# Kernel optimization log

Measured on AMD Instinct MI355X. Metric: run time of the kernel, lower is better.

## Reference

```python
import jax, jax.numpy as jnp
import numpy as np

NUM_EXPERTS = 8
TOP_K = 2
N_EMBD = 1024
D_FFN = 2048  # 4*n_embd//top_k, already multiple of block_size=128


def setup_inputs() -> dict:
    key = jax.random.key(0)
    k1, k2, k3, k4 = jax.random.split(key, 4)
    x = jax.random.normal(k1, (4, 2048, N_EMBD), dtype=jnp.float32)
    router_w = jax.random.normal(k2, (NUM_EXPERTS, N_EMBD), dtype=jnp.float32) * 0.02
    w1 = jax.random.normal(k3, (N_EMBD, D_FFN * NUM_EXPERTS), dtype=jnp.float32) * 0.02
    w2 = jax.random.normal(k4, (D_FFN * NUM_EXPERTS, N_EMBD), dtype=jnp.float32) * 0.02
    return {"x": x, "router_w": router_w, "w1": w1, "w2": w2}


def reference(x, router_w, w1, w2):
    B, T, D = x.shape
    xf = x.reshape(B * T, D)                       # [N, d]
    N = B * T

    # Router: softmax over experts, then top-k selection and renormalization.
    logits = xf @ router_w.T                       # [N, E]
    probs = jax.nn.softmax(logits, axis=-1)
    top_v, top_i = jax.lax.top_k(probs, TOP_K)     # [N, k]
    top_v = top_v / jnp.sum(top_v, axis=-1, keepdims=True)  # norm_topk_prob=True

    # Dense [N, E] routing-weight matrix (zero for non-selected experts).
    gate = jnp.zeros((N, NUM_EXPERTS), dtype=x.dtype)
    gate = gate.at[jnp.arange(N)[:, None], top_i].set(top_v)

    w1r = w1.reshape(D, NUM_EXPERTS, D_FFN)        # expert-major column blocks
    w2r = w2.reshape(NUM_EXPERTS, D_FFN, D)

    out = jnp.zeros((N, D), dtype=x.dtype)
    for e in range(NUM_EXPERTS):
        h = jax.nn.gelu(xf @ w1r[:, e, :], approximate=False)  # [N, f]
        out = out + gate[:, e:e + 1] * (h @ w2r[e])
    return out.reshape(B, T, D)
```

## Files before the change

### kernel.cpp

```cpp
#include <hip/hip_runtime.h>
#include <hip/hip_bf16.h>
#include <cstdint>
#include <cstddef>

#define NE 8
#define N_TOK 8192
#define D_EMB 1024
#define D_FFN 2048

#define BM 128
#define BN 128
#define BK 32

typedef __attribute__((ext_vector_type(8))) short short8;
typedef __attribute__((ext_vector_type(4))) float f32x4;

__device__ __forceinline__ unsigned short f2bf(float f) {
  union { float f; unsigned int u; } c; c.f = f;
  unsigned int u = c.u;
  unsigned int r = u + 0x7FFFu + ((u >> 16) & 1u);
  return (unsigned short)(r >> 16);
}

__device__ __forceinline__ void gll16(const void* g, void* l) {
  __builtin_amdgcn_global_load_lds((const __attribute__((address_space(1))) void*)g,
                                   (__attribute__((address_space(3))) void*)l, 16, 0, 0);
}

__global__ __launch_bounds__(256) void router_k(const float* __restrict__ x,
                                                const float* __restrict__ rw,
                                                int* __restrict__ ti,
                                                float* __restrict__ tg,
                                                ushort* __restrict__ xb) {
  int w = threadIdx.x >> 6, lane = threadIdx.x & 63;
  int n = blockIdx.x * 4 + w;
  const float4* x4 = (const float4*)(x + (size_t)n * D_EMB);
  ushort4* xb4 = (ushort4*)(xb + (size_t)n * D_EMB);
  const float4* r4 = (const float4*)rw;
  float acc[NE];
#pragma unroll
  for (int e = 0; e < NE; ++e) acc[e] = 0.f;
#pragma unroll
  for (int c = 0; c < 4; ++c) {
    float4 xv = x4[c * 64 + lane];
    ushort4 o;
    o.x = f2bf(xv.x); o.y = f2bf(xv.y); o.z = f2bf(xv.z); o.w = f2bf(xv.w);
    xb4[c * 64 + lane] = o;
#pragma unroll
    for (int e = 0; e < NE; ++e) {
      float4 wv = r4[e * 256 + c * 64 + lane];
      acc[e] += xv.x * wv.x + xv.y * wv.y + xv.z * wv.z + xv.w * wv.w;
    }
  }
#pragma unroll
  for (int e = 0; e < NE; ++e) {
    float v = acc[e];
#pragma unroll
    for (int off = 32; off >= 1; off >>= 1) v += __shfl_xor(v, off);
    acc[e] = v;
  }
  if (lane == 0) {
    int e0 = 0; float v0 = acc[0];
#pragma unroll
    for (int e = 1; e < NE; ++e) if (acc[e] > v0) { v0 = acc[e]; e0 = e; }
    int e1 = -1; float v1 = -1e30f;
#pragma unroll
    for (int e = 0; e < NE; ++e) if (e != e0 && acc[e] > v1) { v1 = acc[e]; e1 = e; }
    float p1 = expf(v1 - v0);
    float g0 = 1.f / (1.f + p1);
    float g1 = p1 * g0;
    ti[2 * n] = e0; ti[2 * n + 1] = e1;
    tg[2 * n] = g0; tg[2 * n + 1] = g1;
  }
}

__global__ __launch_bounds__(256) void hist_k(const int* __restrict__ ti,
                                              int* __restrict__ counts) {
  __shared__ int lc[NE];
  if (threadIdx.x < NE) lc[threadIdx.x] = 0;
  __syncthreads();
  int s = blockIdx.x * 512 + threadIdx.x;
  atomicAdd(&lc[ti[s]], 1);
  atomicAdd(&lc[ti[s + 256]], 1);
  __syncthreads();
  if (threadIdx.x < NE) atomicAdd(&counts[threadIdx.x], lc[threadIdx.x]);
}

__global__ void prefix_k(const int* __restrict__ counts, int* __restrict__ bases,
                         int* __restrict__ cursor) {
  if (threadIdx.x == 0) {
    int s = 0;
    for (int e = 0; e < NE; ++e) { bases[e] = s; cursor[e] = s; s += counts[e]; }
  }
}

__global__ __launch_bounds__(256) void scatter_k(const int* __restrict__ ti,
                                                 const float* __restrict__ tg,
                                                 int* __restrict__ cursor,
                                                 int* __restrict__ tok,
                                                 float* __restrict__ gate) {
  __shared__ int lc[NE], lb[NE];
  if (threadIdx.x < NE) lc[threadIdx.x] = 0;
  __syncthreads();
  int s = blockIdx.x * 256 + threadIdx.x;
  int e = ti[s];
  float g = tg[s];
  int loc = atomicAdd(&lc[e], 1);
  __syncthreads();
  if (threadIdx.x < NE) lb[threadIdx.x] = atomicAdd(&cursor[threadIdx.x], lc[threadIdx.x]);
  __syncthreads();
  int pos = lb[e] + loc;
  tok[pos] = s >> 1;
  gate[pos] = g;
}

__global__ __launch_bounds__(256) void transpose_bf_k(const float* __restrict__ src,
                                                      ushort* __restrict__ dst,
                                                      int R, int C) {
  __shared__ ushort t[32][33];
  int bx = blockIdx.x, by = blockIdx.y;
  int rl = threadIdx.x >> 3, q = threadIdx.x & 7;
  float4 v = *(const float4*)&src[(size_t)(by * 32 + rl) * C + bx * 32 + q * 4];
  t[rl][q * 4 + 0] = f2bf(v.x);
  t[rl][q * 4 + 1] = f2bf(v.y);
  t[rl][q * 4 + 2] = f2bf(v.z);
  t[rl][q * 4 + 3] = f2bf(v.w);
  __syncthreads();
  ushort4 o;
  o.x = t[q * 4 + 0][rl];
  o.y = t[q * 4 + 1][rl];
  o.z = t[q * 4 + 2][rl];
  o.w = t[q * 4 + 3][rl];
  *(ushort4*)&dst[(size_t)(bx * 32 + rl) * R + by * 32 + q * 4] = o;
}

__global__ __launch_bounds__(256) void gemm1_k(const ushort* __restrict__ xb,
                                               const ushort* __restrict__ w1t,
                                               const int* __restrict__ counts,
                                               const int* __restrict__ bases,
                                               const int* __restrict__ tok,
                                               ushort* __restrict__ h) {
  int bid = blockIdx.x;
  int e = bid >> 10;
  int rem = bid & 1023;
  int mt = rem >> 4, nt = rem & 15;
  int count = counts[e];
  if (mt * BM >= count) return;
  int base = bases[e];

  __shared__ ushort Al[BM * BK];
  __shared__ ushort Bl[BN * BK];

  int tid = threadIdx.x;
  int w = tid >> 6, lane = tid & 63;

  const ushort* aptr[2]; const ushort* bptr[2];
  ushort* alds[2]; ushort* blds[2];
#pragma unroll
  for (int j = 0; j < 2; ++j) {
    int rl = w * 32 + j * 16 + (lane >> 2);
    int pr = min(base + mt * BM + rl, base + count - 1);
    int t = tok[pr];
    aptr[j] = xb + (size_t)t * D_EMB + (lane & 3) * 8;
    int c = e * D_FFN + nt * BN + rl;
    bptr[j] = w1t + (size_t)c * D_EMB + (lane & 3) * 8;
    alds[j] = Al + (w * 32 + j * 16) * BK;
    blds[j] = Bl + (w * 32 + j * 16) * BK;
  }

  f32x4 zero = {0.f, 0.f, 0.f, 0.f};
  f32x4 acc[4][4];
#pragma unroll
  for (int i = 0; i < 4; ++i)
#pragma unroll
    for (int j = 0; j < 4; ++j) acc[i][j] = zero;

  int wm = w >> 1, wn = w & 1;
  const int arow = (wm * 64 + (lane & 15)) * BK + (lane >> 4) * 8;
  const int brow = (wn * 64 + (lane & 15)) * BK + (lane >> 4) * 8;

  for (int ks = 0; ks < D_EMB / BK; ++ks) {
    __syncthreads();
#pragma unroll
    for (int j = 0; j < 2; ++j) {
      gll16(aptr[j], alds[j]);
      gll16(bptr[j], blds[j]);
      aptr[j] += BK; bptr[j] += BK;
    }
    __syncthreads();
    short8 a[4], b[4];
#pragma unroll
    for (int i = 0; i < 4; ++i) a[i] = *(const short8*)&Al[arow + i * 16 * BK];
#pragma unroll
    for (int j = 0; j < 4; ++j) b[j] = *(const short8*)&Bl[brow + j * 16 * BK];
#pragma unroll
    for (int i = 0; i < 4; ++i)
#pragma unroll
      for (int j = 0; j < 4; ++j)
        acc[i][j] = __builtin_amdgcn_mfma_f32_16x16x32_bf16(a[i], b[j], acc[i][j], 0, 0, 0);
  }

  int r0 = mt * BM + wm * 64, c0 = nt * BN + wn * 64;
#pragma unroll
  for (int i = 0; i < 4; ++i) {
#pragma unroll
    for (int q = 0; q < 4; ++q) {
      int row = r0 + i * 16 + (lane >> 4) * 4 + q;
      if (row < count) {
        size_t hb = (size_t)(base + row) * D_FFN;
#pragma unroll
        for (int j = 0; j < 4; ++j) {
          float v = acc[i][j][q];
          v = 0.5f * v * (1.f + erff(v * 0.70710678118654752f));
          h[hb + c0 + j * 16 + (lane & 15)] = f2bf(v);
        }
      }
    }
  }
}

__global__ __launch_bounds__(256) void gemm2_k(const ushort* __restrict__ h,
                                               const ushort* __restrict__ w2t,
                                               const int* __restrict__ counts,
                                               const int* __restrict__ bases,
                                               const int* __restrict__ tok,
                                               const float* __restrict__ gate,
                                               float* __restrict__ out) {
  int bid = blockIdx.x;
  int e = bid >> 9;
  int rem = bid & 511;
  int mt = rem >> 3, nt = rem & 7;
  int count = counts[e];
  if (mt * BM >= count) return;
  int base = bases[e];

  __shared__ ushort Al[BM * BK];
  __shared__ ushort Bl[BN * BK];

  int tid = threadIdx.x;
  int w = tid >> 6, lane = tid & 63;

  const ushort* aptr[2]; const ushort* bptr[2];
  ushort* alds[2]; ushort* blds[2];
#pragma unroll
  for (int j = 0; j < 2; ++j) {
    int rl = w * 32 + j * 16 + (lane >> 2);
    int pr = min(base + mt * BM + rl, base + count - 1);
    aptr[j] = h + (size_t)pr * D_FFN + (lane & 3) * 8;
    int d = nt * BN + rl;
    bptr[j] = w2t + (size_t)d * (NE * D_FFN) + e * D_FFN + (lane & 3) * 8;
    alds[j] = Al + (w * 32 + j * 16) * BK;
    blds[j] = Bl + (w * 32 + j * 16) * BK;
  }

  f32x4 zero = {0.f, 0.f, 0.f, 0.f};
  f32x4 acc[4][4];
#pragma unroll
  for (int i = 0; i < 4; ++i)
#pragma unroll
    for (int j = 0; j < 4; ++j) acc[i][j] = zero;

  int wm = w >> 1, wn = w & 1;
  const int arow = (wm * 64 + (lane & 15)) * BK + (lane >> 4) * 8;
  const int brow = (wn * 64 + (lane & 15)) * BK + (lane >> 4) * 8;

  for (int ks = 0; ks < D_FFN / BK; ++ks) {
    __syncthreads();
#pragma unroll
    for (int j = 0; j < 2; ++j) {
      gll16(aptr[j], alds[j]);
      gll16(bptr[j], blds[j]);
      aptr[j] += BK; bptr[j] += BK;
    }
    __syncthreads();
    short8 a[4], b[4];
#pragma unroll
    for (int i = 0; i < 4; ++i) a[i] = *(const short8*)&Al[arow + i * 16 * BK];
#pragma unroll
    for (int j = 0; j < 4; ++j) b[j] = *(const short8*)&Bl[brow + j * 16 * BK];
#pragma unroll
    for (int i = 0; i < 4; ++i)
#pragma unroll
      for (int j = 0; j < 4; ++j)
        acc[i][j] = __builtin_amdgcn_mfma_f32_16x16x32_bf16(a[i], b[j], acc[i][j], 0, 0, 0);
  }

  int r0 = mt * BM + wm * 64, c0 = nt * BN + wn * 64;
#pragma unroll
  for (int i = 0; i < 4; ++i) {
#pragma unroll
    for (int q = 0; q < 4; ++q) {
      int row = r0 + i * 16 + (lane >> 4) * 4 + q;
      if (row < count) {
        int pr = base + row;
        int t = tok[pr];
        float g = gate[pr];
        size_t ob = (size_t)t * D_EMB;
#pragma unroll
        for (int j = 0; j < 4; ++j) {
          atomicAdd(&out[ob + c0 + j * 16 + (lane & 15)], g * acc[i][j][q]);
        }
      }
    }
  }
}

extern "C" void kernel_launch(void* const* d_in, const int* in_sizes, int n_in,
                              void* d_out, int out_size, void* d_ws, size_t ws_size,
                              hipStream_t stream) {
  const float* x  = (const float*)d_in[0];
  const float* rw = (const float*)d_in[1];
  const float* w1 = (const float*)d_in[2];
  const float* w2 = (const float*)d_in[3];
  float* out = (float*)d_out;

  char* ws = (char*)d_ws;
  size_t off = 0;
  auto alloc = [&](size_t bytes) {
    void* p = ws + off;
    off = (off + bytes + 255) & ~(size_t)255;
    return p;
  };
  int*    counts = (int*)alloc(32);
  int*    bases  = (int*)alloc(32);
  int*    cursor = (int*)alloc(32);
  int*    ti     = (int*)alloc((size_t)N_TOK * 2 * sizeof(int));
  float*  tg     = (float*)alloc((size_t)N_TOK * 2 * sizeof(float));
  int*    tok    = (int*)alloc((size_t)N_TOK * 2 * sizeof(int));
  float*  gate   = (float*)alloc((size_t)N_TOK * 2 * sizeof(float));
  ushort* xb     = (ushort*)alloc((size_t)N_TOK * D_EMB * 2);
  ushort* w1t    = (ushort*)alloc((size_t)D_EMB * NE * D_FFN * 2);
  ushort* w2t    = (ushort*)alloc((size_t)D_EMB * NE * D_FFN * 2);
  ushort* hbuf   = (ushort*)alloc((size_t)N_TOK * 2 * D_FFN * 2);
  (void)ws_size; (void)in_sizes; (void)n_in;

  hipMemsetAsync(counts, 0, 32, stream);
  hipMemsetAsync(d_out, 0, (size_t)out_size * sizeof(float), stream);

  router_k<<<N_TOK / 4, 256, 0, stream>>>(x, rw, ti, tg, xb);
  transpose_bf_k<<<dim3(512, 32), 256, 0, stream>>>(w1, w1t, D_EMB, NE * D_FFN);
  transpose_bf_k<<<dim3(32, 512), 256, 0, stream>>>(w2, w2t, NE * D_FFN, D_EMB);
  hist_k<<<N_TOK * 2 / 512, 256, 0, stream>>>(ti, counts);
  prefix_k<<<1, 64, 0, stream>>>(counts, bases, cursor);
  scatter_k<<<N_TOK * 2 / 256, 256, 0, stream>>>(ti, tg, cursor, tok, gate);
  gemm1_k<<<NE * 64 * 16, 256, 0, stream>>>(xb, w1t, counts, bases, tok, hbuf);
  gemm2_k<<<NE * 64 * 8, 256, 0, stream>>>(hbuf, w2t, counts, bases, tok, gate, out);
}
```

Measured before the change: 336.4 us.

## Swizzle LDS layout, remap block order per XCD, replace atomic scatter with combine

Applies an XOR swizzle to the LDS tile layout, with matching global source offsets and read offsets, so MFMA operand reads avoid bank conflicts. Remaps block IDs so consecutive blocks are spread across the eight XCDs, which changes which tiles share an L2. gemm2 no longer does fp32 atomicAdd into the output; it writes gated per-slot rows to a bf16 buffer, and a new combine kernel sums each token's two slots using an inverse index built during scatter. This also drops the output memset. The cost is an extra kernel, an intermediate y buffer round trip, and bf16 rounding of the per-expert contributions before they are summed.

```diff
diff --git a/kernel.cpp b/kernel.cpp
--- a/kernel.cpp
+++ b/kernel.cpp
@@ -20,6 +20,11 @@
   unsigned int u = c.u;
   unsigned int r = u + 0x7FFFu + ((u >> 16) & 1u);
   return (unsigned short)(r >> 16);
+}
+
+__device__ __forceinline__ float bf2f(unsigned short u) {
+  union { unsigned int u; float f; } c; c.u = ((unsigned int)u) << 16;
+  return c.f;
 }
 
 __device__ __forceinline__ void gll16(const void* g, void* l) {
@@ -98,7 +103,8 @@
                                                  const float* __restrict__ tg,
                                                  int* __restrict__ cursor,
                                                  int* __restrict__ tok,
-                                                 float* __restrict__ gate) {
+                                                 float* __restrict__ gate,
+                                                 int* __restrict__ inv) {
   __shared__ int lc[NE], lb[NE];
   if (threadIdx.x < NE) lc[threadIdx.x] = 0;
   __syncthreads();
@@ -112,6 +118,7 @@
   int pos = lb[e] + loc;
   tok[pos] = s >> 1;
   gate[pos] = g;
+  inv[s] = pos;
 }
 
 __global__ __launch_bounds__(256) void transpose_bf_k(const float* __restrict__ src,
@@ -134,13 +141,15 @@
   *(ushort4*)&dst[(size_t)(bx * 32 + rl) * R + by * 32 + q * 4] = o;
 }
 
+
 __global__ __launch_bounds__(256) void gemm1_k(const ushort* __restrict__ xb,
                                                const ushort* __restrict__ w1t,
                                                const int* __restrict__ counts,
                                                const int* __restrict__ bases,
                                                const int* __restrict__ tok,
                                                ushort* __restrict__ h) {
-  int bid = blockIdx.x;
+  int bid = (int)blockIdx.x;
+  bid = (bid & 7) * (NE * 1024 / 8) + (bid >> 3);
   int e = bid >> 10;
   int rem = bid & 1023;
   int mt = rem >> 4, nt = rem & 15;
@@ -154,6 +163,8 @@
   int tid = threadIdx.x;
   int w = tid >> 6, lane = tid & 63;
 
+  const int ssw = (((lane & 3) ^ ((lane >> 3) & 3))) * 8;
+
   const ushort* aptr[2]; const ushort* bptr[2];
   ushort* alds[2]; ushort* blds[2];
 #pragma unroll
@@ -161,9 +172,9 @@
     int rl = w * 32 + j * 16 + (lane >> 2);
     int pr = min(base + mt * BM + rl, base + count - 1);
     int t = tok[pr];
-    aptr[j] = xb + (size_t)t * D_EMB + (lane & 3) * 8;
+    aptr[j] = xb + (size_t)t * D_EMB + ssw;
     int c = e * D_FFN + nt * BN + rl;
-    bptr[j] = w1t + (size_t)c * D_EMB + (lane & 3) * 8;
+    bptr[j] = w1t + (size_t)c * D_EMB + ssw;
     alds[j] = Al + (w * 32 + j * 16) * BK;
     blds[j] = Bl + (w * 32 + j * 16) * BK;
   }
@@ -176,8 +187,9 @@
     for (int j = 0; j < 4; ++j) acc[i][j] = zero;
 
   int wm = w >> 1, wn = w & 1;
-  const int arow = (wm * 64 + (lane & 15)) * BK + (lane >> 4) * 8;
-  const int brow = (wn * 64 + (lane & 15)) * BK + (lane >> 4) * 8;
+  const int rsw = ((lane >> 4) ^ (((lane & 15) >> 1) & 3)) * 8;
+  const int arow = (wm * 64 + (lane & 15)) * BK + rsw;
+  const int brow = (wn * 64 + (lane & 15)) * BK + rsw;
 
   for (int ks = 0; ks < D_EMB / BK; ++ks) {
     __syncthreads();
@@ -225,8 +237,9 @@
                                                const int* __restrict__ bases,
                                                const int* __restrict__ tok,
                                                const float* __restrict__ gate,
-                                               float* __restrict__ out) {
-  int bid = blockIdx.x;
+                                               ushort* __restrict__ y) {
+  int bid = (int)blockIdx.x;
+  bid = (bid & 7) * (NE * 512 / 8) + (bid >> 3);
   int e = bid >> 9;
   int rem = bid & 511;
   int mt = rem >> 3, nt = rem & 7;
@@ -240,15 +253,17 @@
   int tid = threadIdx.x;
   int w = tid >> 6, lane = tid & 63;
 
+  const int ssw = (((lane & 3) ^ ((lane >> 3) & 3))) * 8;
+
   const ushort* aptr[2]; const ushort* bptr[2];
   ushort* alds[2]; ushort* blds[2];
 #pragma unroll
   for (int j = 0; j < 2; ++j) {
     int rl = w * 32 + j * 16 + (lane >> 2);
     int pr = min(base + mt * BM + rl, base + count - 1);
-    aptr[j] = h + (size_t)pr * D_FFN + (lane & 3) * 8;
+    aptr[j] = h + (size_t)pr * D_FFN + ssw;
     int d = nt * BN + rl;
-    bptr[j] = w2t + (size_t)d * (NE * D_FFN) + e * D_FFN + (lane & 3) * 8;
+    bptr[j] = w2t + (size_t)d * (NE * D_FFN) + e * D_FFN + ssw;
     alds[j] = Al + (w * 32 + j * 16) * BK;
     blds[j] = Bl + (w * 32 + j * 16) * BK;
   }
@@ -261,8 +276,9 @@
     for (int j = 0; j < 4; ++j) acc[i][j] = zero;
 
   int wm = w >> 1, wn = w & 1;
-  const int arow = (wm * 64 + (lane & 15)) * BK + (lane >> 4) * 8;
-  const int brow = (wn * 64 + (lane & 15)) * BK + (lane >> 4) * 8;
+  const int rsw = ((lane >> 4) ^ (((lane & 15) >> 1) & 3)) * 8;
+  const int arow = (wm * 64 + (lane & 15)) * BK + rsw;
+  const int brow = (wn * 64 + (lane & 15)) * BK + rsw;
 
   for (int ks = 0; ks < D_FFN / BK; ++ks) {
     __syncthreads();
@@ -293,16 +309,33 @@
       int row = r0 + i * 16 + (lane >> 4) * 4 + q;
       if (row < count) {
         int pr = base + row;
-        int t = tok[pr];
         float g = gate[pr];
-        size_t ob = (size_t)t * D_EMB;
+        size_t yb = (size_t)pr * D_EMB;
 #pragma unroll
         for (int j = 0; j < 4; ++j) {
-          atomicAdd(&out[ob + c0 + j * 16 + (lane & 15)], g * acc[i][j][q]);
+          y[yb + c0 + j * 16 + (lane & 15)] = f2bf(g * acc[i][j][q]);
         }
       }
     }
   }
+}
+
+__global__ __launch_bounds__(256) void combine_k(const ushort* __restrict__ y,
+                                                 const int* __restrict__ inv,
+                                                 float* __restrict__ out) {
+  int n = blockIdx.x;
+  int p0 = inv[2 * n], p1 = inv[2 * n + 1];
+  const ushort4* r0 = (const ushort4*)(y + (size_t)p0 * D_EMB);
+  const ushort4* r1 = (const ushort4*)(y + (size_t)p1 * D_EMB);
+  float4* o = (float4*)(out + (size_t)n * D_EMB);
+  int i = threadIdx.x;
+  ushort4 a = r0[i], b = r1[i];
+  float4 v;
+  v.x = bf2f(a.x) + bf2f(b.x);
+  v.y = bf2f(a.y) + bf2f(b.y);
+  v.z = bf2f(a.z) + bf2f(b.z);
+  v.w = bf2f(a.w) + bf2f(b.w);
+  o[i] = v;
 }
 
 extern "C" void kernel_launch(void* const* d_in, const int* in_sizes, int n_in,
@@ -328,21 +361,23 @@
   float*  tg     = (float*)alloc((size_t)N_TOK * 2 * sizeof(float));
   int*    tok    = (int*)alloc((size_t)N_TOK * 2 * sizeof(int));
   float*  gate   = (float*)alloc((size_t)N_TOK * 2 * sizeof(float));
+  int*    inv    = (int*)alloc((size_t)N_TOK * 2 * sizeof(int));
   ushort* xb     = (ushort*)alloc((size_t)N_TOK * D_EMB * 2);
   ushort* w1t    = (ushort*)alloc((size_t)D_EMB * NE * D_FFN * 2);
   ushort* w2t    = (ushort*)alloc((size_t)D_EMB * NE * D_FFN * 2);
   ushort* hbuf   = (ushort*)alloc((size_t)N_TOK * 2 * D_FFN * 2);
-  (void)ws_size; (void)in_sizes; (void)n_in;
+  ushort* ybuf   = (ushort*)alloc((size_t)N_TOK * 2 * D_EMB * 2);
+  (void)ws_size; (void)in_sizes; (void)n_in; (void)out_size;
 
   hipMemsetAsync(counts, 0, 32, stream);
-  hipMemsetAsync(d_out, 0, (size_t)out_size * sizeof(float), stream);
 
   router_k<<<N_TOK / 4, 256, 0, stream>>>(x, rw, ti, tg, xb);
   transpose_bf_k<<<dim3(512, 32), 256, 0, stream>>>(w1, w1t, D_EMB, NE * D_FFN);
   transpose_bf_k<<<dim3(32, 512), 256, 0, stream>>>(w2, w2t, NE * D_FFN, D_EMB);
   hist_k<<<N_TOK * 2 / 512, 256, 0, stream>>>(ti, counts);
   prefix_k<<<1, 64, 0, stream>>>(counts, bases, cursor);
-  scatter_k<<<N_TOK * 2 / 256, 256, 0, stream>>>(ti, tg, cursor, tok, gate);
+  scatter_k<<<N_TOK * 2 / 256, 256, 0, stream>>>(ti, tg, cursor, tok, gate, inv);
   gemm1_k<<<NE * 64 * 16, 256, 0, stream>>>(xb, w1t, counts, bases, tok, hbuf);
-  gemm2_k<<<NE * 64 * 8, 256, 0, stream>>>(hbuf, w2t, counts, bases, tok, gate, out);
-}
+  gemm2_k<<<NE * 64 * 8, 256, 0, stream>>>(hbuf, w2t, counts, bases, tok, gate, ybuf);
+  combine_k<<<N_TOK, 256, 0, stream>>>(ybuf, inv, out);
+}
```

Result: faster. 284.6 us (-15.4%).
